# Optimization experiments

Hardware: AMD Instinct MI355X
Metric: run time of the kernel (lower is better)

## Reference

```python
import jax, jax.numpy as jnp
import numpy as np

L = 32   # latent_dim == enc_dim
ND = 1   # node feature dim (single node type)
B, N = 8, 256
M = 3 * L           # message / Encoder output dim = 2*latent + enc = 96
DIN = 2 * (ND + L) + L  # Encoder input dim = 2*node + 2*latent + enc = 98


def _glorot(key, shape):
    fan_in, fan_out = shape
    s = jnp.sqrt(6.0 / (fan_in + fan_out))
    return jax.random.uniform(key, shape, jnp.float32, -s, s)


def setup_inputs() -> dict:
    key = jax.random.key(0)
    ks = jax.random.split(key, 14)
    return {
        "xs": jax.random.normal(ks[0], (B, N, ND), jnp.float32),
        "hs": jax.random.normal(ks[1], (B, N, L), jnp.float32),
        "e_feat": jax.random.normal(ks[2], (B, N, N, 1), jnp.float32),
        "adj": jax.random.randint(ks[3], (B, N, N), 0, 2, jnp.int32),
        "W_e": _glorot(ks[4], (1, L)),          # edge encoder
        "W_enc_lin": _glorot(ks[5], (DIN, M)),  # Encoder linear branch
        "W_enc_1": _glorot(ks[6], (DIN, M)),    # Encoder non-linear branch
        "W_enc_2": _glorot(ks[7], (M, M)),
        "W_proc_u": _glorot(ks[8], (M, L)),     # processor update
        "W_dec": _glorot(ks[9], (ND + 2 * L, ND)),
        "W_pred": _glorot(ks[10], (2 * L + L, 1)),
        "W_tm": _glorot(ks[11], (2 * L + L, L)),  # termination MPNN message
        "W_tu": _glorot(ks[12], (L, L)),          # termination MPNN update
        "W_term": _glorot(ks[13], (L, 1)),
    }


def reference(xs, hs, adj, e_feat, W_e, W_enc_lin, W_enc_1, W_enc_2,
              W_proc_u, W_dec, W_pred, W_tm, W_tu, W_term):
    b, n = adj.shape[0], adj.shape[1]
    adj2 = adj + jnp.eye(n, dtype=adj.dtype)[None]          # add self-loops
    mask = (adj2 > 0)[..., None]                            # [B,N,N,1]
    neg = jnp.float32(-jnp.inf)

    z = jnp.concatenate([xs, hs], axis=-1)                  # [B,N,ND+L]
    enc_e = jnp.einsum('bije,eh->bijh', e_feat, W_e)        # [B,N,N,L]

    zi = jnp.broadcast_to(z[:, :, None, :], (b, n, n, z.shape[-1]))
    zj = jnp.broadcast_to(z[:, None, :, :], (b, n, n, z.shape[-1]))
    u = jnp.concatenate([zi, zj, enc_e], axis=-1)           # [B,N,N,98]
    # Encoder: linear + 2-layer ReLU MLP (message function)
    msg = u @ W_enc_lin + jax.nn.relu(u @ W_enc_1) @ W_enc_2  # [B,N,N,96]
    agg = jnp.max(jnp.where(mask, msg, neg), axis=2)        # masked max over j
    new_h = agg @ W_proc_u                                  # [B,N,L]

    new_x = jnp.concatenate([z, new_h], axis=-1) @ W_dec    # decoder

    hi = jnp.broadcast_to(new_h[:, :, None, :], (b, n, n, L))
    hj = jnp.broadcast_to(new_h[:, None, :, :], (b, n, n, L))
    hij = jnp.concatenate([hi, hj, enc_e], axis=-1)         # [B,N,N,96]
    p = jnp.where(mask, hij @ W_pred, neg)                  # [B,N,N,1]

    # termination MPNN (tau_in == new_h for single node type)
    mt = jax.nn.relu(hij @ W_tm)                            # [B,N,N,L]
    tau_node = jnp.max(jnp.where(mask, mt, neg), axis=2) @ W_tu
    tau = jnp.mean(tau_node, axis=1) @ W_term               # [B,1]

    cat_h = new_h
    return new_x, p, tau, cat_h
```

## Files before the change

kernel.cpp:

```cpp
#include <hip/hip_runtime.h>
#include <hip/hip_bf16.h>
#include <math.h>

#define BB 8
#define NN 256
#define LLAT 32
#define MM 96
#define ZD 33
#define ROWS (BB*NN)

#define OFF_ALIN   0
#define OFF_BLIN   (OFF_ALIN + ROWS*MM)
#define OFF_A1     (OFF_BLIN + ROWS*MM)
#define OFF_B1     (OFF_A1   + ROWS*MM)
#define OFF_AGG    (OFF_B1   + ROWS*MM)
#define OFF_Z      (OFF_AGG  + ROWS*MM)
#define OFF_NEWH   (OFF_Z    + ROWS*ZD)
#define OFF_PI     (OFF_NEWH + ROWS*LLAT)
#define OFF_PJ     (OFF_PI   + ROWS)
#define OFF_TI     (OFF_PJ   + ROWS)
#define OFF_TJ     (OFF_TI   + ROWS*LLAT)
#define OFF_TAUM   (OFF_TJ   + ROWS*LLAT)
#define OFF_CONST  (OFF_TAUM + ROWS*LLAT)
#define C_LIN   0
#define C_1     96
#define C_PRED  192
#define C_TM    193
#define C_WCOMB 225
#define OFF_W2TH (OFF_CONST + 512)
#define OFF_W2TL (OFF_W2TH + 4992)

#define OUT_NEWX 0
#define OUT_P    2048
#define OUT_TAU  526336
#define OUT_CATH 526344

#define NEG_BIG (-3.0e38f)

typedef __attribute__((ext_vector_type(8))) short bf16x8;
typedef __attribute__((ext_vector_type(4))) float f32x4;

__device__ inline void bf16split(float v, ushort& hi, ushort& lo) {
  __hip_bfloat16 h = __float2bfloat16(v);
  float hf = __bfloat162float(h);
  __hip_bfloat16 l = __float2bfloat16(v - hf);
  hi = *reinterpret_cast<ushort*>(&h);
  lo = *reinterpret_cast<ushort*>(&l);
}

__global__ __launch_bounds__(128) void k_prep(
    const float* __restrict__ xs, const float* __restrict__ hs,
    const float* __restrict__ W_enc_lin, const float* __restrict__ W_enc_1,
    const float* __restrict__ W_e, const float* __restrict__ W_pred,
    const float* __restrict__ W_tm, const float* __restrict__ W_tu,
    const float* __restrict__ W_term, const float* __restrict__ W_enc_2,
    float* __restrict__ ws) {
  int r = blockIdx.x;
  int t = threadIdx.x;
  __shared__ float z[ZD];
  if (t == 0) z[0] = xs[r];
  else if (t < ZD) z[t] = hs[r * LLAT + (t - 1)];
  __syncthreads();
  if (t < ZD) ws[OFF_Z + r * ZD + t] = z[t];
  if (t < 96) {
    float al = 0.f, bl = 0.f, a1 = 0.f, b1 = 0.f;
    #pragma unroll
    for (int k = 0; k < ZD; ++k) {
      float zk = z[k];
      al = fmaf(zk, W_enc_lin[k * 96 + t], al);
      bl = fmaf(zk, W_enc_lin[(ZD + k) * 96 + t], bl);
      a1 = fmaf(zk, W_enc_1[k * 96 + t], a1);
      b1 = fmaf(zk, W_enc_1[(ZD + k) * 96 + t], b1);
    }
    ws[OFF_ALIN + r * 96 + t] = al;
    ws[OFF_BLIN + r * 96 + t] = bl;
    ws[OFF_A1 + r * 96 + t] = a1;
    ws[OFF_B1 + r * 96 + t] = b1;
  }
  if (r < 96) {
    ushort* w2h = (ushort*)(ws + OFF_W2TH);
    ushort* w2l = (ushort*)(ws + OFF_W2TL);
    if (t < 96) {
      ushort hi, lo;
      bf16split(W_enc_2[t * 96 + r], hi, lo);
      w2h[r * 104 + t] = hi;
      w2l[r * 104 + t] = lo;
    }
  } else if (r == 96) {
    float* cst = ws + OFF_CONST;
    if (t < 96) {
      float s0 = 0.f, s1 = 0.f;
      for (int k = 0; k < 32; ++k) {
        float we = W_e[k];
        s0 = fmaf(we, W_enc_lin[(66 + k) * 96 + t], s0);
        s1 = fmaf(we, W_enc_1[(66 + k) * 96 + t], s1);
      }
      cst[C_LIN + t] = s0;
      cst[C_1 + t] = s1;
    }
  } else if (r == 97) {
    float* cst = ws + OFF_CONST;
    if (t < 32) {
      float s_tm = 0.f;
      for (int k = 0; k < 32; ++k) s_tm = fmaf(W_e[k], W_tm[(64 + k) * 32 + t], s_tm);
      cst[C_TM + t] = s_tm;
      float s_wc = 0.f;
      for (int q = 0; q < 32; ++q) s_wc = fmaf(W_tu[t * 32 + q], W_term[q], s_wc);
      cst[C_WCOMB + t] = s_wc;
    } else if (t == 32) {
      float s = 0.f;
      for (int k = 0; k < 32; ++k) s = fmaf(W_e[k], W_pred[64 + k], s);
      cst[C_PRED] = s;
    }
  }
}

__global__ __launch_bounds__(512, 4) void k_main(
    const float* __restrict__ e_feat, const int* __restrict__ adj,
    const float* __restrict__ W_proc_u, const float* __restrict__ W_dec,
    const float* __restrict__ W_pred, const float* __restrict__ W_tm,
    float* __restrict__ ws, float* __restrict__ out) {
  const int bi = blockIdx.x;
  const int i = bi & 255;
  const int brow = bi & ~255;
  const int t = threadIdx.x;
  const int lane = t & 63, w = t >> 6;
  const int l15 = lane & 15, lg = lane >> 4;

  __shared__ __align__(16) ushort W2Ts[2 * 96 * 104];
  __shared__ float A1i[96], ALi[96], c1s[96], cls[96];
  __shared__ float red[8][96];
  __shared__ float aggs[96], nh[32];

  {
    const uint4* src = (const uint4*)(ws + OFF_W2TH);
    uint4* dst = (uint4*)W2Ts;
    for (int idx = t; idx < 2496; idx += 512) dst[idx] = src[idx];
  }
  if (t < 96) {
    A1i[t] = ws[OFF_A1 + bi * 96 + t];
    ALi[t] = ws[OFF_ALIN + bi * 96 + t];
    c1s[t] = ws[OFF_CONST + C_1 + t];
    cls[t] = ws[OFF_CONST + C_LIN + t];
  }

  const int jr0 = w * 32 + l15;
  const int jr1 = jr0 + 16;
  const float* b1base0 = ws + OFF_B1 + (brow + jr0) * 96 + lg * 8;
  const float* b1base1 = ws + OFF_B1 + (brow + jr1) * 96 + lg * 8;
  float4 b1r[2][3][2];
  #pragma unroll
  for (int ks = 0; ks < 3; ++ks) {
    b1r[0][ks][0] = ((const float4*)(b1base0 + ks * 32))[0];
    b1r[0][ks][1] = ((const float4*)(b1base0 + ks * 32))[1];
    b1r[1][ks][0] = ((const float4*)(b1base1 + ks * 32))[0];
    b1r[1][ks][1] = ((const float4*)(b1base1 + ks * 32))[1];
  }
  int adjv[2][4];
  float ejv[2][4];
  #pragma unroll
  for (int jg = 0; jg < 2; ++jg) {
    #pragma unroll
    for (int r = 0; r < 4; ++r) {
      const int j = w * 32 + jg * 16 + lg * 4 + r;
      adjv[jg][r] = adj[bi * 256 + j];
      ejv[jg][r] = e_feat[bi * 256 + j];
    }
  }
  const float ejA0 = e_feat[bi * 256 + jr0];
  const float ejA1 = e_feat[bi * 256 + jr1];

  __syncthreads();

  bf16x8 ah[2][3], al[2][3];
  #pragma unroll
  for (int ks = 0; ks < 3; ++ks) {
    const int ka = ks * 32 + lg * 8;
    float cc[8], aa[8];
    #pragma unroll
    for (int e = 0; e < 4; ++e) {
      cc[e] = c1s[ka + e];      cc[e + 4] = c1s[ka + 4 + e];
      aa[e] = A1i[ka + e];      aa[e + 4] = A1i[ka + 4 + e];
    }
    #pragma unroll
    for (int jg = 0; jg < 2; ++jg) {
      const float ej = jg ? ejA1 : ejA0;
      const float4 b0 = b1r[jg][ks][0], b1 = b1r[jg][ks][1];
      const float vvv[8] = {b0.x, b0.y, b0.z, b0.w, b1.x, b1.y, b1.z, b1.w};
      bf16x8 h8, l8;
      #pragma unroll
      for (int e = 0; e < 8; ++e) {
        float v = fmaxf(fmaf(ej, cc[e], aa[e] + vvv[e]), 0.f);
        ushort hi, lo;
        bf16split(v, hi, lo);
        h8[e] = (short)hi;
        l8[e] = (short)lo;
      }
      ah[jg][ks] = h8;
      al[jg][ks] = l8;
    }
  }

  f32x4 acc[2][6];
  #pragma unroll
  for (int jg = 0; jg < 2; ++jg)
    #pragma unroll
    for (int ct = 0; ct < 6; ++ct) acc[jg][ct] = 0;

  #pragma unroll
  for (int ks = 0; ks < 3; ++ks) {
    const int ka = ks * 32 + lg * 8;
    #pragma unroll
    for (int ct = 0; ct < 6; ++ct) {
      const int br = (ct * 16 + l15) * 104 + ka;
      const bf16x8 bh = *(const bf16x8*)&W2Ts[br];
      const bf16x8 bl = *(const bf16x8*)&W2Ts[96 * 104 + br];
      #pragma unroll
      for (int jg = 0; jg < 2; ++jg) {
        acc[jg][ct] = __builtin_amdgcn_mfma_f32_16x16x32_bf16(ah[jg][ks], bh, acc[jg][ct], 0, 0, 0);
        acc[jg][ct] = __builtin_amdgcn_mfma_f32_16x16x32_bf16(ah[jg][ks], bl, acc[jg][ct], 0, 0, 0);
        acc[jg][ct] = __builtin_amdgcn_mfma_f32_16x16x32_bf16(al[jg][ks], bh, acc[jg][ct], 0, 0, 0);
      }
    }
  }

  float aliC[6], clsC[6];
  #pragma unroll
  for (int ct = 0; ct < 6; ++ct) {
    const int c = ct * 16 + l15;
    aliC[ct] = ALi[c];
    clsC[ct] = cls[c];
  }
  float rmax[6] = {-INFINITY, -INFINITY, -INFINITY, -INFINITY, -INFINITY, -INFINITY};
  #pragma unroll
  for (int jg = 0; jg < 2; ++jg) {
    #pragma unroll
    for (int r = 0; r < 4; ++r) {
      const int j = w * 32 + jg * 16 + lg * 4 + r;
      const bool msk = (adjv[jg][r] > 0) || (j == i);
      if (msk) {
        const float ej = ejv[jg][r];
        const float* BL = ws + OFF_BLIN + (brow + j) * 96;
        #pragma unroll
        for (int ct = 0; ct < 6; ++ct) {
          float val = acc[jg][ct][r] + aliC[ct] + fmaf(clsC[ct], ej, BL[ct * 16 + l15]);
          rmax[ct] = fmaxf(rmax[ct], val);
        }
      }
    }
  }

  #pragma unroll
  for (int ct = 0; ct < 6; ++ct) {
    float v = rmax[ct];
    v = fmaxf(v, __shfl_xor(v, 16));
    v = fmaxf(v, __shfl_xor(v, 32));
    rmax[ct] = v;
  }
  if (lg == 0) {
    #pragma unroll
    for (int ct = 0; ct < 6; ++ct) red[w][ct * 16 + l15] = rmax[ct];
  }
  __syncthreads();
  if (t < 96) {
    float m = red[0][t];
    #pragma unroll
    for (int q = 1; q < 8; ++q) m = fmaxf(m, red[q][t]);
    aggs[t] = m;
  }
  __syncthreads();

  if (t < 32) {
    float s = 0.f;
    #pragma unroll 8
    for (int c = 0; c < 96; ++c) s = fmaf(aggs[c], W_proc_u[c * 32 + t], s);
    nh[t] = s;
    out[OUT_CATH + bi * 32 + t] = s;
  }
  __syncthreads();
  if (t < 32) {
    float si = 0.f, sj = 0.f;
    #pragma unroll
    for (int m = 0; m < 32; ++m) {
      si = fmaf(nh[m], W_tm[m * 32 + t], si);
      sj = fmaf(nh[m], W_tm[(32 + m) * 32 + t], sj);
    }
    ws[OFF_TI + bi * 32 + t] = si;
    ws[OFF_TJ + bi * 32 + t] = sj;
  } else if (t == 32) {
    float s = 0.f;
    for (int k = 0; k < ZD; ++k) s = fmaf(ws[OFF_Z + bi * ZD + k], W_dec[k], s);
    for (int m = 0; m < 32; ++m) s = fmaf(nh[m], W_dec[ZD + m], s);
    out[OUT_NEWX + bi] = s;
  } else if (t == 33) {
    float s = 0.f;
    for (int m = 0; m < 32; ++m) s = fmaf(nh[m], W_pred[m], s);
    ws[OFF_PI + bi] = s;
  } else if (t == 34) {
    float s = 0.f;
    for (int m = 0; m < 32; ++m) s = fmaf(nh[m], W_pred[32 + m], s);
    ws[OFF_PJ + bi] = s;
  }
  if (bi < 8 && t == 36) out[OUT_TAU + bi] = 0.f;
}

__global__ __launch_bounds__(256) void k_pair(
    const float* __restrict__ e_feat, const int* __restrict__ adj,
    float* __restrict__ ws, float* __restrict__ out) {
  int bi = blockIdx.x;
  int i = bi & 255;
  int brow = bi & ~255;
  int t = threadIdx.x;
  __shared__ float Tis[32], ctms[32], partial[8][32];
  __shared__ float Pis, cpred;
  if (t < 32) {
    Tis[t] = ws[OFF_TI + bi * 32 + t];
    ctms[t] = ws[OFF_CONST + C_TM + t];
  } else if (t == 32) {
    Pis = ws[OFF_PI + bi];
  } else if (t == 33) {
    cpred = ws[OFF_CONST + C_PRED];
  }
  __syncthreads();

  {
    const int j = t;
    float ej = e_feat[bi * 256 + j];
    bool msk = (adj[bi * 256 + j] > 0) || (j == i);
    float pv = msk ? (Pis + ws[OFF_PJ + brow + j] + ej * cpred) : NEG_BIG;
    out[OUT_P + bi * 256 + j] = pv;
  }

  {
    const int k = t & 31, g = t >> 5;
    const float tik = Tis[k], ctk = ctms[k];
    const float* Tj = ws + OFF_TJ + brow * 32;
    float m = -INFINITY;
    #pragma unroll 4
    for (int jj = 0; jj < 32; ++jj) {
      const int j = g * 32 + jj;
      float tjv = Tj[j * 32 + k];
      float ejj = e_feat[bi * 256 + j];
      bool mk = (adj[bi * 256 + j] > 0) || (j == i);
      float val = fmaxf(tik + fmaf(ejj, ctk, tjv), 0.f);
      m = mk ? fmaxf(m, val) : m;
    }
    partial[g][k] = m;
  }
  __syncthreads();
  if (t < 32) {
    float v = partial[0][t];
    #pragma unroll
    for (int g = 1; g < 8; ++g) v = fmaxf(v, partial[g][t]);
    float s = v * ws[OFF_CONST + C_WCOMB + t];
    s += __shfl_xor(s, 1);
    s += __shfl_xor(s, 2);
    s += __shfl_xor(s, 4);
    s += __shfl_xor(s, 8);
    s += __shfl_xor(s, 16);
    if (t == 0) atomicAdd(&out[OUT_TAU + (bi >> 8)], s * (1.0f / 256.0f));
  }
}

extern "C" void kernel_launch(void* const* d_in, const int* in_sizes, int n_in,
                              void* d_out, int out_size, void* d_ws, size_t ws_size,
                              hipStream_t stream) {
  const float* xs        = (const float*)d_in[0];
  const float* hs        = (const float*)d_in[1];
  const float* e_feat    = (const float*)d_in[2];
  const int*   adj       = (const int*)d_in[3];
  const float* W_e       = (const float*)d_in[4];
  const float* W_enc_lin = (const float*)d_in[5];
  const float* W_enc_1   = (const float*)d_in[6];
  const float* W_enc_2   = (const float*)d_in[7];
  const float* W_proc_u  = (const float*)d_in[8];
  const float* W_dec     = (const float*)d_in[9];
  const float* W_pred    = (const float*)d_in[10];
  const float* W_tm      = (const float*)d_in[11];
  const float* W_tu      = (const float*)d_in[12];
  const float* W_term    = (const float*)d_in[13];

  float* ws  = (float*)d_ws;
  float* out = (float*)d_out;

  k_prep<<<ROWS, 128, 0, stream>>>(xs, hs, W_enc_lin, W_enc_1, W_e, W_pred,
                                   W_tm, W_tu, W_term, W_enc_2, ws);
  k_main<<<ROWS, 512, 0, stream>>>(e_feat, adj, W_proc_u, W_dec, W_pred, W_tm,
                                   ws, out);
  k_pair<<<ROWS, 256, 0, stream>>>(e_feat, adj, ws, out);
}
```

Before: 187.0 us.

## Batch prep rows per block, parallelize tail dot products, stage pair rows in LDS

k_prep now processes 8 rows per block and first stages the z-related W_enc_lin/W_enc_1 weights in shared memory. The grid shrinks from 2048 blocks to 264, which cuts repeated global weight reads; the W_enc_2 transpose and tau zeroing move into dedicated blocks. In k_main the single-thread serial dot products for new_x and the pred terms become wavefront shuffle reductions. In k_pair, e_feat, the mask and P_j are loaded once into LDS and reused across all eight groups instead of being re-read from global memory in the inner loop. The cost is about 50 KB of LDS per k_prep block.

```diff
diff --git a/kernel.cpp b/kernel.cpp
--- a/kernel.cpp
+++ b/kernel.cpp
@@ -48,45 +48,74 @@
   lo = *reinterpret_cast<ushort*>(&l);
 }
 
-__global__ __launch_bounds__(128) void k_prep(
+__global__ __launch_bounds__(256) void k_prep(
     const float* __restrict__ xs, const float* __restrict__ hs,
     const float* __restrict__ W_enc_lin, const float* __restrict__ W_enc_1,
     const float* __restrict__ W_e, const float* __restrict__ W_pred,
     const float* __restrict__ W_tm, const float* __restrict__ W_tu,
     const float* __restrict__ W_term, const float* __restrict__ W_enc_2,
-    float* __restrict__ ws) {
-  int r = blockIdx.x;
-  int t = threadIdx.x;
-  __shared__ float z[ZD];
-  if (t == 0) z[0] = xs[r];
-  else if (t < ZD) z[t] = hs[r * LLAT + (t - 1)];
-  __syncthreads();
-  if (t < ZD) ws[OFF_Z + r * ZD + t] = z[t];
-  if (t < 96) {
-    float al = 0.f, bl = 0.f, a1 = 0.f, b1 = 0.f;
-    #pragma unroll
-    for (int k = 0; k < ZD; ++k) {
-      float zk = z[k];
-      al = fmaf(zk, W_enc_lin[k * 96 + t], al);
-      bl = fmaf(zk, W_enc_lin[(ZD + k) * 96 + t], bl);
-      a1 = fmaf(zk, W_enc_1[k * 96 + t], a1);
-      b1 = fmaf(zk, W_enc_1[(ZD + k) * 96 + t], b1);
-    }
-    ws[OFF_ALIN + r * 96 + t] = al;
-    ws[OFF_BLIN + r * 96 + t] = bl;
-    ws[OFF_A1 + r * 96 + t] = a1;
-    ws[OFF_B1 + r * 96 + t] = b1;
-  }
-  if (r < 96) {
+    float* __restrict__ ws, float* __restrict__ out) {
+  const int blk = blockIdx.x;
+  const int t = threadIdx.x;
+
+  if (blk < 256) {
+    const int r0 = blk * 8;
+    __shared__ float WzL[66 * 96];
+    __shared__ float Wz1[66 * 96];
+    __shared__ float zz[8][34];
+    {
+      const uint4* sL = (const uint4*)W_enc_lin;
+      const uint4* s1 = (const uint4*)W_enc_1;
+      uint4* dL = (uint4*)WzL;
+      uint4* d1 = (uint4*)Wz1;
+      for (int idx = t; idx < 1584; idx += 256) {
+        dL[idx] = sL[idx];
+        d1[idx] = s1[idx];
+      }
+    }
+    {
+      const int r = t >> 5, e = t & 31;
+      zz[r][e + 1] = hs[(r0 + r) * 32 + e];
+      if (t < 8) zz[t][0] = xs[r0 + t];
+    }
+    __syncthreads();
+    for (int idx = t; idx < 8 * ZD; idx += 256) {
+      const int r = idx / ZD, e = idx - r * ZD;
+      ws[OFF_Z + (r0 + r) * ZD + e] = zz[r][e];
+    }
+    const int r = t >> 5;
+    const int gr = r0 + r;
+    #pragma unroll
+    for (int q = 0; q < 3; ++q) {
+      const int c = (t & 31) + 32 * q;
+      float al = 0.f, bl = 0.f, a1 = 0.f, b1 = 0.f;
+      #pragma unroll
+      for (int k = 0; k < ZD; ++k) {
+        const float zk = zz[r][k];
+        al = fmaf(zk, WzL[k * 96 + c], al);
+        bl = fmaf(zk, WzL[(ZD + k) * 96 + c], bl);
+        a1 = fmaf(zk, Wz1[k * 96 + c], a1);
+        b1 = fmaf(zk, Wz1[(ZD + k) * 96 + c], b1);
+      }
+      ws[OFF_ALIN + gr * 96 + c] = al;
+      ws[OFF_BLIN + gr * 96 + c] = bl;
+      ws[OFF_A1 + gr * 96 + c] = a1;
+      ws[OFF_B1 + gr * 96 + c] = b1;
+    }
+  } else if (blk < 262) {
+    const int c = (blk - 256) * 16 + (t >> 4);
+    const int kk0 = (t & 15) * 6;
     ushort* w2h = (ushort*)(ws + OFF_W2TH);
     ushort* w2l = (ushort*)(ws + OFF_W2TL);
-    if (t < 96) {
+    #pragma unroll
+    for (int q = 0; q < 6; ++q) {
+      const int kk = kk0 + q;
       ushort hi, lo;
-      bf16split(W_enc_2[t * 96 + r], hi, lo);
-      w2h[r * 104 + t] = hi;
-      w2l[r * 104 + t] = lo;
-    }
-  } else if (r == 96) {
+      bf16split(W_enc_2[kk * 96 + c], hi, lo);
+      w2h[c * 104 + kk] = hi;
+      w2l[c * 104 + kk] = lo;
+    }
+  } else if (blk == 262) {
     float* cst = ws + OFF_CONST;
     if (t < 96) {
       float s0 = 0.f, s1 = 0.f;
@@ -98,7 +127,7 @@
       cst[C_LIN + t] = s0;
       cst[C_1 + t] = s1;
     }
-  } else if (r == 97) {
+  } else {
     float* cst = ws + OFF_CONST;
     if (t < 32) {
       float s_tm = 0.f;
@@ -111,6 +140,8 @@
       float s = 0.f;
       for (int k = 0; k < 32; ++k) s = fmaf(W_e[k], W_pred[64 + k], s);
       cst[C_PRED] = s;
+    } else if (t >= 40 && t < 48) {
+      out[OUT_TAU + (t - 40)] = 0.f;
     }
   }
 }
@@ -287,32 +318,47 @@
     }
     ws[OFF_TI + bi * 32 + t] = si;
     ws[OFF_TJ + bi * 32 + t] = sj;
-  } else if (t == 32) {
-    float s = 0.f;
-    for (int k = 0; k < ZD; ++k) s = fmaf(ws[OFF_Z + bi * ZD + k], W_dec[k], s);
-    for (int m = 0; m < 32; ++m) s = fmaf(nh[m], W_dec[ZD + m], s);
-    out[OUT_NEWX + bi] = s;
-  } else if (t == 33) {
-    float s = 0.f;
-    for (int m = 0; m < 32; ++m) s = fmaf(nh[m], W_pred[m], s);
-    ws[OFF_PI + bi] = s;
-  } else if (t == 34) {
-    float s = 0.f;
-    for (int m = 0; m < 32; ++m) s = fmaf(nh[m], W_pred[32 + m], s);
-    ws[OFF_PJ + bi] = s;
-  }
-  if (bi < 8 && t == 36) out[OUT_TAU + bi] = 0.f;
+  } else if (t >= 64 && t < 128) {
+    const int idx = t - 64;
+    float v = 0.f;
+    if (idx < ZD) v = ws[OFF_Z + bi * ZD + idx] * W_dec[idx];
+    else if (idx < ZD + 32) v = nh[idx - ZD] * W_dec[idx];
+    v += __shfl_xor(v, 1);
+    v += __shfl_xor(v, 2);
+    v += __shfl_xor(v, 4);
+    v += __shfl_xor(v, 8);
+    v += __shfl_xor(v, 16);
+    v += __shfl_xor(v, 32);
+    if (idx == 0) out[OUT_NEWX + bi] = v;
+  } else if (t >= 128 && t < 192) {
+    const int idx = t - 128;
+    const int m = idx & 31;
+    float v = nh[m] * W_pred[idx];
+    v += __shfl_xor(v, 1);
+    v += __shfl_xor(v, 2);
+    v += __shfl_xor(v, 4);
+    v += __shfl_xor(v, 8);
+    v += __shfl_xor(v, 16);
+    if (idx == 0) ws[OFF_PI + bi] = v;
+    else if (idx == 32) ws[OFF_PJ + bi] = v;
+  }
 }
 
 __global__ __launch_bounds__(256) void k_pair(
     const float* __restrict__ e_feat, const int* __restrict__ adj,
     float* __restrict__ ws, float* __restrict__ out) {
-  int bi = blockIdx.x;
-  int i = bi & 255;
-  int brow = bi & ~255;
-  int t = threadIdx.x;
+  const int bi = blockIdx.x;
+  const int i = bi & 255;
+  const int brow = bi & ~255;
+  const int t = threadIdx.x;
   __shared__ float Tis[32], ctms[32], partial[8][32];
+  __shared__ float ejr[256], pjr[256];
+  __shared__ int mskr[256];
   __shared__ float Pis, cpred;
+
+  ejr[t] = e_feat[bi * 256 + t];
+  pjr[t] = ws[OFF_PJ + brow + t];
+  mskr[t] = (adj[bi * 256 + t] > 0) || (t == i);
   if (t < 32) {
     Tis[t] = ws[OFF_TI + bi * 32 + t];
     ctms[t] = ws[OFF_CONST + C_TM + t];
@@ -323,27 +369,20 @@
   }
   __syncthreads();
 
-  {
-    const int j = t;
-    float ej = e_feat[bi * 256 + j];
-    bool msk = (adj[bi * 256 + j] > 0) || (j == i);
-    float pv = msk ? (Pis + ws[OFF_PJ + brow + j] + ej * cpred) : NEG_BIG;
-    out[OUT_P + bi * 256 + j] = pv;
-  }
+  out[OUT_P + bi * 256 + t] =
+      mskr[t] ? (Pis + pjr[t] + ejr[t] * cpred) : NEG_BIG;
 
   {
     const int k = t & 31, g = t >> 5;
     const float tik = Tis[k], ctk = ctms[k];
     const float* Tj = ws + OFF_TJ + brow * 32;
     float m = -INFINITY;
-    #pragma unroll 4
+    #pragma unroll
     for (int jj = 0; jj < 32; ++jj) {
       const int j = g * 32 + jj;
-      float tjv = Tj[j * 32 + k];
-      float ejj = e_feat[bi * 256 + j];
-      bool mk = (adj[bi * 256 + j] > 0) || (j == i);
-      float val = fmaxf(tik + fmaf(ejj, ctk, tjv), 0.f);
-      m = mk ? fmaxf(m, val) : m;
+      const float tjv = Tj[j * 32 + k];
+      const float val = fmaxf(tik + fmaf(ejr[j], ctk, tjv), 0.f);
+      m = mskr[j] ? fmaxf(m, val) : m;
     }
     partial[g][k] = m;
   }
@@ -383,8 +422,8 @@
   float* ws  = (float*)d_ws;
   float* out = (float*)d_out;
 
-  k_prep<<<ROWS, 128, 0, stream>>>(xs, hs, W_enc_lin, W_enc_1, W_e, W_pred,
-                                   W_tm, W_tu, W_term, W_enc_2, ws);
+  k_prep<<<264, 256, 0, stream>>>(xs, hs, W_enc_lin, W_enc_1, W_e, W_pred,
+                                  W_tm, W_tu, W_term, W_enc_2, ws, out);
   k_main<<<ROWS, 512, 0, stream>>>(e_feat, adj, W_proc_u, W_dec, W_pred, W_tm,
                                    ws, out);
   k_pair<<<ROWS, 256, 0, stream>>>(e_feat, adj, ws, out);
```

New measurement: 182.3 us. 1.03x faster.
